# Performance work log

Measured on AMD Instinct MI355X. Metric: run time of the kernel, lower is better.

The kernel has to match this reference:

```python
import jax, jax.numpy as jnp
import numpy as np

NEG = -65504.0  # torch.finfo(float16).min
EPS = 1e-6

B, T, D = 2, 1024, 2048
H, HD = 16, 128          # n_head, head_dim
K = 128                  # dynamic_w_hidden_dim
IH = 1                   # dynamic_hidden_dim = H // squeeze_ratio


def _rope(x, freqs_cis):
    # x: [B,T,H,hd]; 'half' mode: first/second half are the rotation pair,
    # output is interleaved (stack(...,-1).flatten(3) in torch).
    half = x.shape[-1] // 2
    a, b = x[..., :half], x[..., half:]
    cos = freqs_cis[None, :, None, :, 0]
    sin = freqs_cis[None, :, None, :, 1]
    out = jnp.stack([a * cos - b * sin, b * cos + a * sin], axis=-1)
    return out.reshape(x.shape)


def _cross_head_proj(inputs, qw1, qw2, kw1, kw2, qdd, kdd):
    # inputs: [B,N,T,S]; qw1/qw2: [B,T,I,N]; kw1/kw2: [B,S,I,N]; qdd: [B,T,N]; kdd: [B,S,N]
    out = inputs
    out = out + jnp.einsum('bnts,btin,btim->bmts', inputs, qw1, qw2)
    out = out + jnp.einsum('bnts,bsin,bsim->bmts', inputs, kw1, kw2)
    out = out + inputs * jnp.swapaxes(qdd, 1, 2)[..., None]   # [B,N,T,1]
    out = out + inputs * jnp.swapaxes(kdd, 1, 2)[:, :, None, :]  # [B,N,1,S]
    return out


def setup_inputs() -> dict:
    key = jax.random.key(0)
    ks = jax.random.split(key, 7)
    x = jax.random.normal(ks[0], (B, T, D), jnp.float32)
    mask = jnp.tril(jnp.ones((1, 1, T, T), bool))  # causal
    # rotary tables: [T, hd/2, 2] (cos, sin)
    inv = 1.0 / (10000.0 ** (jnp.arange(0, HD, 2, dtype=jnp.float32) / HD))
    ang = jnp.arange(T, dtype=jnp.float32)[:, None] * inv[None, :]
    freqs_cis = jnp.stack([jnp.cos(ang), jnp.sin(ang)], axis=-1)
    s = 0.02
    wqkv = jax.random.normal(ks[1], (D, 3 * H * HD), jnp.float32) * s
    wo = jax.random.normal(ks[2], (H * HD, D), jnp.float32) * s
    dw1 = jax.random.normal(ks[3], (D, 4, K), jnp.float32) * s
    qkw = jax.random.normal(ks[4], (4, K, 2 * IH, H), jnp.float32) * s
    dd_w = jax.random.normal(ks[5], (D, 4 * H), jnp.float32) * s
    return {"x": x, "mask": mask, "freqs_cis": freqs_cis, "wqkv": wqkv,
            "wo": wo, "dw1": dw1, "qkw": qkw, "dd_w": dd_w}


def reference(x, mask, freqs_cis, wqkv, wo, dw1, qkw, dd_w):
    b, t, d = x.shape
    qkv = x @ wqkv
    q, k, v = jnp.split(qkv, [H * HD, 2 * H * HD], axis=-1)
    q = q.reshape(b, t, H, HD)
    k = k.reshape(b, t, H, HD)
    v = v.reshape(b, t, H, HD)
    q = _rope(q, freqs_cis)
    k = _rope(k, freqs_cis)
    q = jnp.swapaxes(q, 1, 2) * (HD ** -0.5)  # [B,H,T,hd]
    k = jnp.swapaxes(k, 1, 2)
    v = jnp.swapaxes(v, 1, 2)

    # ---- DynamicWeightProjection (G=1, squeezed) ----
    dw_hidden = jax.nn.gelu(jnp.einsum('btd,dck->btck', x, dw1), approximate=False)
    w = jnp.einsum('btck,ckim->btcim', dw_hidden, qkw)  # [B,T,4,2*IH,H]
    w1, w2 = w[..., :IH, :], w[..., IH:, :]
    w1 = w1 * jax.lax.rsqrt(jnp.mean(w1 * w1, axis=-1, keepdims=True) + EPS)
    pre_qw1, pre_kw1, post_qw1, post_kw1 = [w1[:, :, i] for i in range(4)]
    pre_qw2, pre_kw2, post_qw2, post_kw2 = [w2[:, :, i] for i in range(4)]
    dd = jnp.tanh(x @ dd_w).reshape(b, t, 4, H)
    pre_qdd, pre_kdd, post_qdd, post_kdd = [dd[:, :, i] for i in range(4)]

    # ---- attention with cross-head mixing ----
    logits = jnp.einsum('bhtd,bhsd->bhts', q, k)
    logits = _cross_head_proj(logits, pre_qw1, pre_qw2, pre_kw1, pre_kw2, pre_qdd, pre_kdd)
    logits = jnp.where(mask, logits, NEG)
    probs = jax.nn.softmax(logits, axis=-1)
    probs = _cross_head_proj(probs, post_qw1, post_qw2, post_kw1, post_kw2, post_qdd, post_kdd)
    o = jnp.einsum('bhts,bhsd->bhtd', probs, v)
    o = jnp.swapaxes(o, 1, 2).reshape(b, t, H * HD)
    return o @ wo
```

## Files before the change

kernel.cpp:

```cpp
#include <hip/hip_runtime.h>


typedef unsigned short u16;
typedef unsigned int u32;
typedef __attribute__((ext_vector_type(8))) short s16x8;
typedef __attribute__((ext_vector_type(4))) float f32x4;
typedef __attribute__((ext_vector_type(2))) float f32x2;
typedef __attribute__((ext_vector_type(2))) u16 u16x2;

#define DEV __device__ __forceinline__

DEV float bf2f(u16 u) { union { u32 u; float f; } a; a.u = ((u32)u) << 16; return a.f; }
DEV u16 f2bf(float f) {
  union { float f; u32 u; } a; a.f = f;
  u32 r = a.u + 0x7fffu + ((a.u >> 16) & 1u);
  return (u16)(r >> 16);
}

DEV void gload16(const void* g, void* l) {
  __builtin_amdgcn_global_load_lds((__attribute__((address_space(1))) void*)g,
                                   (__attribute__((address_space(3))) void*)l,
                                   16, 0, 0);
}

template <int OUTBF>
__global__ __launch_bounds__(256) void gemm_bt(
    const u16* __restrict__ A, const u16* __restrict__ B, void* __restrict__ Cp,
    int K, int lda, int ldb, int ldc,
    long sAb, long sBb, long sCb1, long sCb2, int CZ2, int cmode, int swz)
{
  int bx = blockIdx.x, by = blockIdx.y;
  if (swz) {
    int nx = gridDim.x;
    int fid = by * nx + bx;
    int cpx = (nx * gridDim.y) >> 3;
    int nid = (fid & 7) * cpx + (fid >> 3);
    bx = nid % nx; by = nid / nx;
  }
  if (cmode == 1 && bx > by) return;
  __shared__ u16 sA[128 * 64];
  __shared__ u16 sB[128 * 64];
  const int tid = threadIdx.x, wv = tid >> 6, ln = tid & 63;
  const int z = blockIdx.z;
  const u16* Ab = A + (size_t)z * sAb + (size_t)(by * 128) * lda;
  const u16* Bb = B + (size_t)z * sBb + (size_t)(bx * 128) * ldb;
  const int wr = (wv >> 1) * 64, wc = (wv & 1) * 64;
  const int Keff = (cmode == 2) ? min(K, (by + 1) * 128) : K;

  f32x4 acc[4][4];
#pragma unroll
  for (int m = 0; m < 4; ++m)
#pragma unroll
    for (int n = 0; n < 4; ++n) {
      f32x4 zz = {0.f, 0.f, 0.f, 0.f};
      acc[m][n] = zz;
    }

  int o_[4], r_[4], cb_[4];
#pragma unroll
  for (int i = 0; i < 4; ++i) {
    int o = (wv * 4 + i) * 1024 + ln * 16;
    o_[i] = o;
    int r = o >> 7;
    r_[i] = r;
    cb_[i] = (o & 127) ^ ((r & 7) << 4);
  }
  const int frswz = (ln & 7) << 4;
  const int fkcol = (ln >> 4) << 4;

  for (int k0 = 0; k0 < Keff; k0 += 64) {
    __syncthreads();
#pragma unroll
    for (int i = 0; i < 4; ++i)
      gload16(Ab + (size_t)r_[i] * lda + (k0 + (cb_[i] >> 1)), (char*)sA + o_[i]);
#pragma unroll
    for (int i = 0; i < 4; ++i)
      gload16(Bb + (size_t)r_[i] * ldb + (k0 + (cb_[i] >> 1)), (char*)sB + o_[i]);
    __syncthreads();

#pragma unroll
    for (int ks = 0; ks < 2; ++ks) {
      s16x8 av[4], bv[4];
#pragma unroll
      for (int m = 0; m < 4; ++m) {
        int row = wr + m * 16 + (ln & 15);
        int addr = row * 128 + ((ks * 64 + fkcol) ^ frswz);
        av[m] = *(const s16x8*)((const char*)sA + addr);
      }
#pragma unroll
      for (int n = 0; n < 4; ++n) {
        int row = wc + n * 16 + (ln & 15);
        int addr = row * 128 + ((ks * 64 + fkcol) ^ frswz);
        bv[n] = *(const s16x8*)((const char*)sB + addr);
      }
#pragma unroll
      for (int m = 0; m < 4; ++m)
#pragma unroll
        for (int n = 0; n < 4; ++n)
          acc[m][n] = __builtin_amdgcn_mfma_f32_16x16x32_bf16(av[m], bv[n], acc[m][n], 0, 0, 0);
    }
  }

  const size_t cbase = (size_t)(z / CZ2) * sCb1 + (size_t)(z % CZ2) * sCb2;
  const int r0 = by * 128 + wr + ((ln >> 4) << 2);
  const int c0 = bx * 128 + wc + (ln & 15);
#pragma unroll
  for (int m = 0; m < 4; ++m)
#pragma unroll
    for (int n = 0; n < 4; ++n)
#pragma unroll
      for (int j = 0; j < 4; ++j) {
        int row = r0 + m * 16 + j, col = c0 + n * 16;
        if (OUTBF)
          ((u16*)Cp)[cbase + (size_t)row * ldc + col] = f2bf(acc[m][n][j]);
        else
          ((float*)Cp)[cbase + (size_t)row * ldc + col] = acc[m][n][j];
      }
}

template <int INBF>
__global__ __launch_bounds__(256) void transpose_to_bf16(
    const void* __restrict__ srcv, u16* __restrict__ dst,
    int R, int C, int Cpad, int srcLd, long sSrc1, long sSrc2, int Z2, long sDst)
{
  __shared__ float tile[32][33];
  const int z = blockIdx.z, z1 = z / Z2, z2 = z % Z2;
  const size_t sbase = (size_t)z1 * sSrc1 + (size_t)z2 * sSrc2;
  u16* d = dst + (size_t)z * sDst;
  const int c0 = blockIdx.x * 32, r0 = blockIdx.y * 32;
  const int tx = threadIdx.x, ty = threadIdx.y;
#pragma unroll
  for (int i = 0; i < 4; ++i) {
    int r = r0 + ty + i * 8, c = c0 + tx;
    float v = 0.f;
    if (c < C && r < R) {
      if (INBF) v = bf2f(((const u16*)srcv)[sbase + (size_t)r * srcLd + c]);
      else      v = ((const float*)srcv)[sbase + (size_t)r * srcLd + c];
    }
    tile[ty + i * 8][tx] = v;
  }
  __syncthreads();
#pragma unroll
  for (int i = 0; i < 4; ++i) {
    int dr = c0 + ty + i * 8, dc = r0 + tx;
    if (dr < Cpad && dc < R) d[(size_t)dr * R + dc] = f2bf(tile[tx][ty + i * 8]);
  }
}

__global__ void cvt_f32_bf16_k(const float* __restrict__ src, u16* __restrict__ dst, int n4) {
  int i = blockIdx.x * 256 + threadIdx.x;
  if (i >= n4) return;
  const float4 v = ((const float4*)src)[i];
  u16* o = dst + (size_t)i * 4;
  o[0] = f2bf(v.x); o[1] = f2bf(v.y); o[2] = f2bf(v.z); o[3] = f2bf(v.w);
}

__global__ __launch_bounds__(256) void rope_k(
    const u16* __restrict__ qkvb, const float* __restrict__ fc,
    u16* __restrict__ qb, u16* __restrict__ kb)
{
  const int bt = blockIdx.x, b = bt >> 10, t = bt & 1023;
  const u16* row = qkvb + (size_t)bt * 6144;
  const float SC = 0.08838834764831845f;
#pragma unroll
  for (int it = 0; it < 4; ++it) {
    int idx = threadIdx.x + it * 256;
    int h = idx >> 6, j = idx & 63;
    float c = fc[(t * 64 + j) * 2], sn = fc[(t * 64 + j) * 2 + 1];
    float qa = bf2f(row[h * 128 + j]), qbv = bf2f(row[h * 128 + 64 + j]);
    float ka = bf2f(row[2048 + h * 128 + j]), kbv = bf2f(row[2048 + h * 128 + 64 + j]);
    size_t o = ((size_t)(b * 16 + h) * 1024 + t) * 128 + 2 * j;
    qb[o]     = f2bf((qa * c - qbv * sn) * SC);
    qb[o + 1] = f2bf((qbv * c + qa * sn) * SC);
    kb[o]     = f2bf(ka * c - kbv * sn);
    kb[o + 1] = f2bf(kbv * c + ka * sn);
  }
}

__global__ __launch_bounds__(128) void gelu_k(float* __restrict__ hm) {
  int bt = blockIdx.x, tid = threadIdx.x;
  float* p = hm + (size_t)bt * 640 + tid * 4;
  float4 v = *(float4*)p;
  v.x = 0.5f * v.x * (1.f + erff(v.x * 0.70710678118654752f));
  v.y = 0.5f * v.y * (1.f + erff(v.y * 0.70710678118654752f));
  v.z = 0.5f * v.z * (1.f + erff(v.z * 0.70710678118654752f));
  v.w = 0.5f * v.w * (1.f + erff(v.w * 0.70710678118654752f));
  *(float4*)p = v;
}

__global__ __launch_bounds__(64) void wproj_k(
    const float* __restrict__ hid, const float* __restrict__ qkw,
    float* __restrict__ w1a, float* __restrict__ w2a, float* __restrict__ kpT)
{
  const int bt = blockIdx.x, ln = threadIdx.x;
  const int c = ln >> 4, m = ln & 15;
  const int b = bt >> 10, t = bt & 1023;
  const float* hp = hid + (size_t)bt * 640 + c * 128;
  const float* Wp = qkw + (size_t)c * 4096 + m;
  float w1 = 0.f, w2 = 0.f;
  for (int k = 0; k < 128; ++k) {
    float hv = hp[k];
    w1 += hv * Wp[k * 32];
    w2 += hv * Wp[k * 32 + 16];
  }
  float ss = w1 * w1;
  ss += __shfl_xor(ss, 1); ss += __shfl_xor(ss, 2);
  ss += __shfl_xor(ss, 4); ss += __shfl_xor(ss, 8);
  float nrm = rsqrtf(ss * (1.f / 16.f) + 1e-6f);
  float w1n = w1 * nrm;
  size_t o = (size_t)bt * 64 + c * 16 + m;
  w1a[o] = w1n;
  w2a[o] = w2;
  size_t kb = (size_t)b * 98304 + (size_t)m * 1024 + t;
  if (c == 1) { kpT[kb] = w1n; kpT[kb + 16384] = w2; }
  if (c == 3) { kpT[kb + 49152] = w1n; kpT[kb + 65536] = w2; }
}

__global__ __launch_bounds__(64) void dd_k(const float* __restrict__ hm,
                                           float* __restrict__ dda, float* __restrict__ kpT) {
  int bt = blockIdx.x, ln = threadIdx.x;
  int c = ln >> 4, m = ln & 15;
  int b = bt >> 10, t = bt & 1023;
  float v = tanhf(hm[(size_t)bt * 640 + 512 + ln]);
  dda[(size_t)bt * 64 + ln] = v;
  size_t kb = (size_t)b * 98304 + (size_t)m * 1024 + t;
  if (c == 1) kpT[kb + 32768] = v;
  if (c == 3) kpT[kb + 81920] = v;
}

__global__ __launch_bounds__(512, 4) void proj_softmax_k(
    const float* __restrict__ L, u16* __restrict__ P,
    const float* __restrict__ w1a, const float* __restrict__ w2a,
    const float* __restrict__ dda, const float* __restrict__ kparT)
{
  const int t = blockIdx.x, b = blockIdx.y;
  const int tid = threadIdx.x, wv = tid >> 6, ln = tid & 63;
  const int s0 = tid * 2;
  const bool live = (s0 <= t);

  __shared__ float qpar[6][16];
  __shared__ float red2[16][8];
  __shared__ float rzf[16];
  if (tid < 96) {
    int a = tid >> 4, hh = tid & 15;
    const float* sp = (a == 0 || a == 3) ? w1a : ((a == 1 || a == 4) ? w2a : dda);
    int cc = (a < 3) ? 0 : 2;
    qpar[a][hh] = sp[(size_t)(b * 1024 + t) * 64 + cc * 16 + hh];
  }
  __syncthreads();

  const float* kp = kparT + (size_t)b * 98304 + s0;
  float v[16][2];
  const size_t lbase = ((size_t)(b * 16) * 1024 + t) * 1024 + s0;

  if (live) {
#pragma unroll
    for (int h = 0; h < 16; ++h) {
      f32x2 d = *(const f32x2*)(L + lbase + (size_t)h * 1048576);
      v[h][0] = d[0]; v[h][1] = d[1];
    }
    float dq0 = 0.f, dq1 = 0.f, dk0 = 0.f, dk1 = 0.f;
#pragma unroll
    for (int h = 0; h < 16; ++h) {
      f32x2 k1 = *(const f32x2*)(kp + h * 1024);
      dq0 += v[h][0] * qpar[0][h]; dq1 += v[h][1] * qpar[0][h];
      dk0 += v[h][0] * k1[0];      dk1 += v[h][1] * k1[1];
    }
    const bool ok1 = (s0 + 1 <= t);
#pragma unroll
    for (int h = 0; h < 16; ++h) {
      f32x2 k2 = *(const f32x2*)(kp + 16384 + h * 1024);
      f32x2 kd = *(const f32x2*)(kp + 32768 + h * 1024);
      float a0 = v[h][0] * (1.f + qpar[2][h] + kd[0]) + qpar[1][h] * dq0 + k2[0] * dk0;
      float a1 = v[h][1] * (1.f + qpar[2][h] + kd[1]) + qpar[1][h] * dq1 + k2[1] * dk1;
      v[h][0] = __expf(a0);
      v[h][1] = ok1 ? __expf(a1) : 0.f;
    }
  }

#pragma unroll
  for (int h = 0; h < 16; ++h) {
    float x = live ? (v[h][0] + v[h][1]) : 0.f;
#pragma unroll
    for (int off = 32; off > 0; off >>= 1) x += __shfl_xor(x, off);
    if (ln == 0) red2[h][wv] = x;
  }
  __syncthreads();
  if (tid < 16)
    rzf[tid] = 1.f / (((red2[tid][0] + red2[tid][1]) + (red2[tid][2] + red2[tid][3])) +
                      ((red2[tid][4] + red2[tid][5]) + (red2[tid][6] + red2[tid][7])));
  __syncthreads();

  const size_t pbase = ((size_t)(b * 16) * 1024 + t) * 1024 + s0;
  if (live) {
    float pdq0 = 0.f, pdq1 = 0.f, pdk0 = 0.f, pdk1 = 0.f;
#pragma unroll
    for (int h = 0; h < 16; ++h) {
      float rz = rzf[h];
      f32x2 k1 = *(const f32x2*)(kp + 49152 + h * 1024);
      float p0 = v[h][0] * rz, p1 = v[h][1] * rz;
      v[h][0] = p0; v[h][1] = p1;
      pdq0 += p0 * qpar[3][h]; pdq1 += p1 * qpar[3][h];
      pdk0 += p0 * k1[0];      pdk1 += p1 * k1[1];
    }
#pragma unroll
    for (int h = 0; h < 16; ++h) {
      f32x2 k2 = *(const f32x2*)(kp + 65536 + h * 1024);
      f32x2 kd = *(const f32x2*)(kp + 81920 + h * 1024);
      u16x2 pk;
      pk[0] = f2bf(v[h][0] * (1.f + qpar[5][h] + kd[0]) + qpar[4][h] * pdq0 + k2[0] * pdk0);
      pk[1] = f2bf(v[h][1] * (1.f + qpar[5][h] + kd[1]) + qpar[4][h] * pdq1 + k2[1] * pdk1);
      *(u16x2*)(P + pbase + (size_t)h * 1048576) = pk;
    }
  } else {
    u16x2 z2 = {0, 0};
#pragma unroll
    for (int h = 0; h < 16; ++h)
      *(u16x2*)(P + pbase + (size_t)h * 1048576) = z2;
  }
}

extern "C" void kernel_launch(void* const* d_in, const int* in_sizes, int n_in,
                              void* d_out, int out_size, void* d_ws, size_t ws_size,
                              hipStream_t stream)
{
  (void)in_sizes; (void)n_in; (void)out_size; (void)ws_size;
  const float* x    = (const float*)d_in[0];
  const float* fc   = (const float*)d_in[2];
  const float* wqkv = (const float*)d_in[3];
  const float* wo   = (const float*)d_in[4];
  const float* dw1  = (const float*)d_in[5];
  const float* qkw  = (const float*)d_in[6];
  const float* ddw  = (const float*)d_in[7];
  float* out = (float*)d_out;
  char* w = (char*)d_ws;

  u16*   woT   = (u16*)(w + 0);
  u16*   qb    = (u16*)(w + 8388608);
  u16*   kb    = (u16*)(w + 16777216);
  u16*   vT    = (u16*)(w + 25165824);
  u16*   obf   = (u16*)(w + 33554432);
  float* w1a   = (float*)(w + 41943040);
  float* w2a   = (float*)(w + 42467328);
  float* dda   = (float*)(w + 42991616);
  const size_t TB = 43515904;
  u16*   xb    = (u16*)(w + TB);
  u16*   wqkvT = (u16*)(w + TB + 8388608);
  u16*   dwddT = (u16*)(w + TB + 33554432);
  u16*   qkvb  = (u16*)(w + TB + 36175872);
  float* hidm  = (float*)(w + TB + 61341696);
  float* L     = (float*)(w + TB);
  u16*   P     = (u16*)(w + TB + 134217728);
  float* kparT = (float*)(w + 244842496);

  cvt_f32_bf16_k<<<4096, 256, 0, stream>>>(x, xb, 1048576);
  transpose_to_bf16<0><<<dim3(192, 64, 1), dim3(32, 8), 0, stream>>>(wqkv, wqkvT, 2048, 6144, 6144, 6144, 0, 0, 1, 0);
  transpose_to_bf16<0><<<dim3(16, 64, 1),  dim3(32, 8), 0, stream>>>(dw1,  dwddT, 2048, 512,  512,  512,  0, 0, 1, 0);
  transpose_to_bf16<0><<<dim3(4, 64, 1),   dim3(32, 8), 0, stream>>>(ddw,  dwddT + 512 * 2048, 2048, 64, 128, 64, 0, 0, 1, 0);
  transpose_to_bf16<0><<<dim3(64, 64, 1),  dim3(32, 8), 0, stream>>>(wo,   woT,   2048, 2048, 2048, 2048, 0, 0, 1, 0);

  gemm_bt<1><<<dim3(48, 16, 1), 256, 0, stream>>>(xb, wqkvT, qkvb, 2048, 2048, 2048, 6144, 0, 0, 0, 0, 1, 0, 1);
  rope_k<<<2048, 256, 0, stream>>>(qkvb, fc, qb, kb);
  transpose_to_bf16<1><<<dim3(4, 32, 32), dim3(32, 8), 0, stream>>>(qkvb + 4096, vT, 1024, 128, 128, 6144, 6291456, 128, 16, 131072);

  gemm_bt<0><<<dim3(5, 16, 1), 256, 0, stream>>>(xb, dwddT, hidm, 2048, 2048, 2048, 640, 0, 0, 0, 0, 1, 0, 0);
  gelu_k<<<2048, 128, 0, stream>>>(hidm);
  wproj_k<<<2048, 64, 0, stream>>>(hidm, qkw, w1a, w2a, kparT);
  dd_k<<<2048, 64, 0, stream>>>(hidm, dda, kparT);

  gemm_bt<0><<<dim3(8, 8, 32), 256, 0, stream>>>(qb, kb, L, 128, 128, 128, 1024, 131072, 131072, 1048576, 0, 1, 1, 0);
  proj_softmax_k<<<dim3(1024, 2, 1), 512, 0, stream>>>(L, P, w1a, w2a, dda, kparT);
  gemm_bt<1><<<dim3(1, 8, 32), 256, 0, stream>>>(P, vT, obf, 1024, 1024, 1024, 2048, 1048576, 131072, 2097152, 128, 16, 2, 0);

  gemm_bt<0><<<dim3(16, 16, 1), 256, 0, stream>>>(obf, woT, out, 2048, 2048, 2048, 2048, 0, 0, 0, 0, 1, 0, 1);
}
```

Baseline: 336.9 us.

## Fuse dynamic-weight GEMM into QKV GEMM and process two query rows per softmax block

The dw1 and dd_w weight transposes now sit next to wqkv, so one GEMM with N=6784 produces QKV plus the dynamic hidden pre-activations in bf16. This removes the separate small GEMM launch and its poor occupancy, and gelu, wproj and dd now read that bf16 output. The proj_softmax kernel now handles two query rows per block, which halves the block count and reuses the key-side parameter loads across both rows. In exchange, the hidden activations are rounded to bf16 before gelu, and each thread holds more registers.

```diff
diff --git a/kernel.cpp b/kernel.cpp
--- a/kernel.cpp
+++ b/kernel.cpp
@@ -7,6 +7,7 @@
 typedef __attribute__((ext_vector_type(4))) float f32x4;
 typedef __attribute__((ext_vector_type(2))) float f32x2;
 typedef __attribute__((ext_vector_type(2))) u16 u16x2;
+typedef __attribute__((ext_vector_type(8))) u16 u16x8;
 
 #define DEV __device__ __forceinline__
 
@@ -156,11 +157,11 @@
 }
 
 __global__ __launch_bounds__(256) void rope_k(
-    const u16* __restrict__ qkvb, const float* __restrict__ fc,
+    const u16* __restrict__ qkvm, const float* __restrict__ fc,
     u16* __restrict__ qb, u16* __restrict__ kb)
 {
   const int bt = blockIdx.x, b = bt >> 10, t = bt & 1023;
-  const u16* row = qkvb + (size_t)bt * 6144;
+  const u16* row = qkvm + (size_t)bt * 6784;
   const float SC = 0.08838834764831845f;
 #pragma unroll
   for (int it = 0; it < 4; ++it) {
@@ -177,29 +178,31 @@
   }
 }
 
-__global__ __launch_bounds__(128) void gelu_k(float* __restrict__ hm) {
+__global__ __launch_bounds__(64) void gelu_bf16_k(u16* __restrict__ qm) {
   int bt = blockIdx.x, tid = threadIdx.x;
-  float* p = hm + (size_t)bt * 640 + tid * 4;
-  float4 v = *(float4*)p;
-  v.x = 0.5f * v.x * (1.f + erff(v.x * 0.70710678118654752f));
-  v.y = 0.5f * v.y * (1.f + erff(v.y * 0.70710678118654752f));
-  v.z = 0.5f * v.z * (1.f + erff(v.z * 0.70710678118654752f));
-  v.w = 0.5f * v.w * (1.f + erff(v.w * 0.70710678118654752f));
-  *(float4*)p = v;
+  u16* p = qm + (size_t)bt * 6784 + 6144 + tid * 8;
+  u16x8 v = *(u16x8*)p;
+#pragma unroll
+  for (int i = 0; i < 8; ++i) {
+    float f = bf2f(v[i]);
+    f = 0.5f * f * (1.f + erff(f * 0.70710678118654752f));
+    v[i] = f2bf(f);
+  }
+  *(u16x8*)p = v;
 }
 
 __global__ __launch_bounds__(64) void wproj_k(
-    const float* __restrict__ hid, const float* __restrict__ qkw,
+    const u16* __restrict__ qkvm, const float* __restrict__ qkw,
     float* __restrict__ w1a, float* __restrict__ w2a, float* __restrict__ kpT)
 {
   const int bt = blockIdx.x, ln = threadIdx.x;
   const int c = ln >> 4, m = ln & 15;
   const int b = bt >> 10, t = bt & 1023;
-  const float* hp = hid + (size_t)bt * 640 + c * 128;
+  const u16* hp = qkvm + (size_t)bt * 6784 + 6144 + c * 128;
   const float* Wp = qkw + (size_t)c * 4096 + m;
   float w1 = 0.f, w2 = 0.f;
   for (int k = 0; k < 128; ++k) {
-    float hv = hp[k];
+    float hv = bf2f(hp[k]);
     w1 += hv * Wp[k * 32];
     w2 += hv * Wp[k * 32 + 16];
   }
@@ -216,12 +219,12 @@
   if (c == 3) { kpT[kb + 49152] = w1n; kpT[kb + 65536] = w2; }
 }
 
-__global__ __launch_bounds__(64) void dd_k(const float* __restrict__ hm,
+__global__ __launch_bounds__(64) void dd_k(const u16* __restrict__ qkvm,
                                            float* __restrict__ dda, float* __restrict__ kpT) {
   int bt = blockIdx.x, ln = threadIdx.x;
   int c = ln >> 4, m = ln & 15;
   int b = bt >> 10, t = bt & 1023;
-  float v = tanhf(hm[(size_t)bt * 640 + 512 + ln]);
+  float v = tanhf(bf2f(qkvm[(size_t)bt * 6784 + 6656 + ln]));
   dda[(size_t)bt * 64 + ln] = v;
   size_t kb = (size_t)b * 98304 + (size_t)m * 1024 + t;
   if (c == 1) kpT[kb + 32768] = v;
@@ -233,90 +236,121 @@
     const float* __restrict__ w1a, const float* __restrict__ w2a,
     const float* __restrict__ dda, const float* __restrict__ kparT)
 {
-  const int t = blockIdx.x, b = blockIdx.y;
+  const int t0 = blockIdx.x * 2, b = blockIdx.y;
   const int tid = threadIdx.x, wv = tid >> 6, ln = tid & 63;
   const int s0 = tid * 2;
-  const bool live = (s0 <= t);
-
-  __shared__ float qpar[6][16];
-  __shared__ float red2[16][8];
-  __shared__ float rzf[16];
-  if (tid < 96) {
-    int a = tid >> 4, hh = tid & 15;
+  const bool liveB = (s0 <= t0 + 1);
+
+  __shared__ float qpar[2][6][16];
+  __shared__ float red2[2][16][8];
+  __shared__ float rzf[2][16];
+  if (tid < 192) {
+    int tt = (tid >= 96) ? 1 : 0, u = tid - tt * 96;
+    int a = u >> 4, hh = u & 15;
     const float* sp = (a == 0 || a == 3) ? w1a : ((a == 1 || a == 4) ? w2a : dda);
     int cc = (a < 3) ? 0 : 2;
-    qpar[a][hh] = sp[(size_t)(b * 1024 + t) * 64 + cc * 16 + hh];
+    qpar[tt][a][hh] = sp[(size_t)(b * 1024 + t0 + tt) * 64 + cc * 16 + hh];
   }
   __syncthreads();
 
   const float* kp = kparT + (size_t)b * 98304 + s0;
-  float v[16][2];
-  const size_t lbase = ((size_t)(b * 16) * 1024 + t) * 1024 + s0;
-
-  if (live) {
-#pragma unroll
-    for (int h = 0; h < 16; ++h) {
-      f32x2 d = *(const f32x2*)(L + lbase + (size_t)h * 1048576);
-      v[h][0] = d[0]; v[h][1] = d[1];
-    }
-    float dq0 = 0.f, dq1 = 0.f, dk0 = 0.f, dk1 = 0.f;
+  float vA[16][2], vB[16][2];
+  const size_t lbaseA = ((size_t)(b * 16) * 1024 + t0) * 1024 + s0;
+  const size_t lbaseB = lbaseA + 1024;
+
+  if (liveB) {
+#pragma unroll
+    for (int h = 0; h < 16; ++h) {
+      f32x2 dA = *(const f32x2*)(L + lbaseA + (size_t)h * 1048576);
+      f32x2 dB = *(const f32x2*)(L + lbaseB + (size_t)h * 1048576);
+      vA[h][0] = dA[0]; vA[h][1] = dA[1];
+      vB[h][0] = dB[0]; vB[h][1] = dB[1];
+    }
+    float dqA0 = 0.f, dqA1 = 0.f, dkA0 = 0.f, dkA1 = 0.f;
+    float dqB0 = 0.f, dqB1 = 0.f, dkB0 = 0.f, dkB1 = 0.f;
 #pragma unroll
     for (int h = 0; h < 16; ++h) {
       f32x2 k1 = *(const f32x2*)(kp + h * 1024);
-      dq0 += v[h][0] * qpar[0][h]; dq1 += v[h][1] * qpar[0][h];
-      dk0 += v[h][0] * k1[0];      dk1 += v[h][1] * k1[1];
-    }
-    const bool ok1 = (s0 + 1 <= t);
+      dqA0 += vA[h][0] * qpar[0][0][h]; dqA1 += vA[h][1] * qpar[0][0][h];
+      dkA0 += vA[h][0] * k1[0];         dkA1 += vA[h][1] * k1[1];
+      dqB0 += vB[h][0] * qpar[1][0][h]; dqB1 += vB[h][1] * qpar[1][0][h];
+      dkB0 += vB[h][0] * k1[0];         dkB1 += vB[h][1] * k1[1];
+    }
+    const bool okA0 = (s0 <= t0), okA1 = (s0 + 1 <= t0), okB1 = (s0 + 1 <= t0 + 1);
 #pragma unroll
     for (int h = 0; h < 16; ++h) {
       f32x2 k2 = *(const f32x2*)(kp + 16384 + h * 1024);
       f32x2 kd = *(const f32x2*)(kp + 32768 + h * 1024);
-      float a0 = v[h][0] * (1.f + qpar[2][h] + kd[0]) + qpar[1][h] * dq0 + k2[0] * dk0;
-      float a1 = v[h][1] * (1.f + qpar[2][h] + kd[1]) + qpar[1][h] * dq1 + k2[1] * dk1;
-      v[h][0] = __expf(a0);
-      v[h][1] = ok1 ? __expf(a1) : 0.f;
+      float aA0 = vA[h][0] * (1.f + qpar[0][2][h] + kd[0]) + qpar[0][1][h] * dqA0 + k2[0] * dkA0;
+      float aA1 = vA[h][1] * (1.f + qpar[0][2][h] + kd[1]) + qpar[0][1][h] * dqA1 + k2[1] * dkA1;
+      float aB0 = vB[h][0] * (1.f + qpar[1][2][h] + kd[0]) + qpar[1][1][h] * dqB0 + k2[0] * dkB0;
+      float aB1 = vB[h][1] * (1.f + qpar[1][2][h] + kd[1]) + qpar[1][1][h] * dqB1 + k2[1] * dkB1;
+      vA[h][0] = okA0 ? __expf(aA0) : 0.f;
+      vA[h][1] = okA1 ? __expf(aA1) : 0.f;
+      vB[h][0] = __expf(aB0);
+      vB[h][1] = okB1 ? __expf(aB1) : 0.f;
+    }
+  } else {
+#pragma unroll
+    for (int h = 0; h < 16; ++h) {
+      vA[h][0] = 0.f; vA[h][1] = 0.f; vB[h][0] = 0.f; vB[h][1] = 0.f;
     }
   }
 
 #pragma unroll
   for (int h = 0; h < 16; ++h) {
-    float x = live ? (v[h][0] + v[h][1]) : 0.f;
-#pragma unroll
-    for (int off = 32; off > 0; off >>= 1) x += __shfl_xor(x, off);
-    if (ln == 0) red2[h][wv] = x;
+    float xA = vA[h][0] + vA[h][1];
+    float xB = vB[h][0] + vB[h][1];
+#pragma unroll
+    for (int off = 32; off > 0; off >>= 1) {
+      xA += __shfl_xor(xA, off);
+      xB += __shfl_xor(xB, off);
+    }
+    if (ln == 0) { red2[0][h][wv] = xA; red2[1][h][wv] = xB; }
   }
   __syncthreads();
-  if (tid < 16)
-    rzf[tid] = 1.f / (((red2[tid][0] + red2[tid][1]) + (red2[tid][2] + red2[tid][3])) +
-                      ((red2[tid][4] + red2[tid][5]) + (red2[tid][6] + red2[tid][7])));
+  if (tid < 32) {
+    int tt = tid >> 4, h = tid & 15;
+    rzf[tt][h] = 1.f / (((red2[tt][h][0] + red2[tt][h][1]) + (red2[tt][h][2] + red2[tt][h][3])) +
+                        ((red2[tt][h][4] + red2[tt][h][5]) + (red2[tt][h][6] + red2[tt][h][7])));
+  }
   __syncthreads();
 
-  const size_t pbase = ((size_t)(b * 16) * 1024 + t) * 1024 + s0;
-  if (live) {
-    float pdq0 = 0.f, pdq1 = 0.f, pdk0 = 0.f, pdk1 = 0.f;
-#pragma unroll
-    for (int h = 0; h < 16; ++h) {
-      float rz = rzf[h];
+  const size_t pbaseA = lbaseA, pbaseB = lbaseB;
+  if (liveB) {
+    float pdqA0 = 0.f, pdqA1 = 0.f, pdkA0 = 0.f, pdkA1 = 0.f;
+    float pdqB0 = 0.f, pdqB1 = 0.f, pdkB0 = 0.f, pdkB1 = 0.f;
+#pragma unroll
+    for (int h = 0; h < 16; ++h) {
       f32x2 k1 = *(const f32x2*)(kp + 49152 + h * 1024);
-      float p0 = v[h][0] * rz, p1 = v[h][1] * rz;
-      v[h][0] = p0; v[h][1] = p1;
-      pdq0 += p0 * qpar[3][h]; pdq1 += p1 * qpar[3][h];
-      pdk0 += p0 * k1[0];      pdk1 += p1 * k1[1];
+      float rzA = rzf[0][h], rzB = rzf[1][h];
+      float pA0 = vA[h][0] * rzA, pA1 = vA[h][1] * rzA;
+      float pB0 = vB[h][0] * rzB, pB1 = vB[h][1] * rzB;
+      vA[h][0] = pA0; vA[h][1] = pA1; vB[h][0] = pB0; vB[h][1] = pB1;
+      pdqA0 += pA0 * qpar[0][3][h]; pdqA1 += pA1 * qpar[0][3][h];
+      pdkA0 += pA0 * k1[0];         pdkA1 += pA1 * k1[1];
+      pdqB0 += pB0 * qpar[1][3][h]; pdqB1 += pB1 * qpar[1][3][h];
+      pdkB0 += pB0 * k1[0];         pdkB1 += pB1 * k1[1];
     }
 #pragma unroll
     for (int h = 0; h < 16; ++h) {
       f32x2 k2 = *(const f32x2*)(kp + 65536 + h * 1024);
       f32x2 kd = *(const f32x2*)(kp + 81920 + h * 1024);
-      u16x2 pk;
-      pk[0] = f2bf(v[h][0] * (1.f + qpar[5][h] + kd[0]) + qpar[4][h] * pdq0 + k2[0] * pdk0);
-      pk[1] = f2bf(v[h][1] * (1.f + qpar[5][h] + kd[1]) + qpar[4][h] * pdq1 + k2[1] * pdk1);
-      *(u16x2*)(P + pbase + (size_t)h * 1048576) = pk;
+      u16x2 pkA, pkB;
+      pkA[0] = f2bf(vA[h][0] * (1.f + qpar[0][5][h] + kd[0]) + qpar[0][4][h] * pdqA0 + k2[0] * pdkA0);
+      pkA[1] = f2bf(vA[h][1] * (1.f + qpar[0][5][h] + kd[1]) + qpar[0][4][h] * pdqA1 + k2[1] * pdkA1);
+      pkB[0] = f2bf(vB[h][0] * (1.f + qpar[1][5][h] + kd[0]) + qpar[1][4][h] * pdqB0 + k2[0] * pdkB0);
+      pkB[1] = f2bf(vB[h][1] * (1.f + qpar[1][5][h] + kd[1]) + qpar[1][4][h] * pdqB1 + k2[1] * pdkB1);
+      *(u16x2*)(P + pbaseA + (size_t)h * 1048576) = pkA;
+      *(u16x2*)(P + pbaseB + (size_t)h * 1048576) = pkB;
     }
   } else {
     u16x2 z2 = {0, 0};
 #pragma unroll
-    for (int h = 0; h < 16; ++h)
-      *(u16x2*)(P + pbase + (size_t)h * 1048576) = z2;
+    for (int h = 0; h < 16; ++h) {
+      *(u16x2*)(P + pbaseA + (size_t)h * 1048576) = z2;
+      *(u16x2*)(P + pbaseB + (size_t)h * 1048576) = z2;
+    }
   }
 }
 
@@ -345,31 +379,28 @@
   float* dda   = (float*)(w + 42991616);
   const size_t TB = 43515904;
   u16*   xb    = (u16*)(w + TB);
-  u16*   wqkvT = (u16*)(w + TB + 8388608);
-  u16*   dwddT = (u16*)(w + TB + 33554432);
-  u16*   qkvb  = (u16*)(w + TB + 36175872);
-  float* hidm  = (float*)(w + TB + 61341696);
+  u16*   wallT = (u16*)(w + TB + 8388608);
+  u16*   qkvm  = (u16*)(w + TB + 36175872);
   float* L     = (float*)(w + TB);
   u16*   P     = (u16*)(w + TB + 134217728);
   float* kparT = (float*)(w + 244842496);
 
   cvt_f32_bf16_k<<<4096, 256, 0, stream>>>(x, xb, 1048576);
-  transpose_to_bf16<0><<<dim3(192, 64, 1), dim3(32, 8), 0, stream>>>(wqkv, wqkvT, 2048, 6144, 6144, 6144, 0, 0, 1, 0);
-  transpose_to_bf16<0><<<dim3(16, 64, 1),  dim3(32, 8), 0, stream>>>(dw1,  dwddT, 2048, 512,  512,  512,  0, 0, 1, 0);
-  transpose_to_bf16<0><<<dim3(4, 64, 1),   dim3(32, 8), 0, stream>>>(ddw,  dwddT + 512 * 2048, 2048, 64, 128, 64, 0, 0, 1, 0);
-  transpose_to_bf16<0><<<dim3(64, 64, 1),  dim3(32, 8), 0, stream>>>(wo,   woT,   2048, 2048, 2048, 2048, 0, 0, 1, 0);
-
-  gemm_bt<1><<<dim3(48, 16, 1), 256, 0, stream>>>(xb, wqkvT, qkvb, 2048, 2048, 2048, 6144, 0, 0, 0, 0, 1, 0, 1);
-  rope_k<<<2048, 256, 0, stream>>>(qkvb, fc, qb, kb);
-  transpose_to_bf16<1><<<dim3(4, 32, 32), dim3(32, 8), 0, stream>>>(qkvb + 4096, vT, 1024, 128, 128, 6144, 6291456, 128, 16, 131072);
-
-  gemm_bt<0><<<dim3(5, 16, 1), 256, 0, stream>>>(xb, dwddT, hidm, 2048, 2048, 2048, 640, 0, 0, 0, 0, 1, 0, 0);
-  gelu_k<<<2048, 128, 0, stream>>>(hidm);
-  wproj_k<<<2048, 64, 0, stream>>>(hidm, qkw, w1a, w2a, kparT);
-  dd_k<<<2048, 64, 0, stream>>>(hidm, dda, kparT);
+  transpose_to_bf16<0><<<dim3(192, 64, 1), dim3(32, 8), 0, stream>>>(wqkv, wallT, 2048, 6144, 6144, 6144, 0, 0, 1, 0);
+  transpose_to_bf16<0><<<dim3(16, 64, 1),  dim3(32, 8), 0, stream>>>(dw1,  wallT + (size_t)6144 * 2048, 2048, 512, 512, 512, 0, 0, 1, 0);
+  transpose_to_bf16<0><<<dim3(4, 64, 1),   dim3(32, 8), 0, stream>>>(ddw,  wallT + (size_t)6656 * 2048, 2048, 64, 128, 64, 0, 0, 1, 0);
+  transpose_to_bf16<0><<<dim3(64, 64, 1),  dim3(32, 8), 0, stream>>>(wo,   woT, 2048, 2048, 2048, 2048, 0, 0, 1, 0);
+
+  gemm_bt<1><<<dim3(53, 16, 1), 256, 0, stream>>>(xb, wallT, qkvm, 2048, 2048, 2048, 6784, 0, 0, 0, 0, 1, 0, 1);
+  rope_k<<<2048, 256, 0, stream>>>(qkvm, fc, qb, kb);
+  transpose_to_bf16<1><<<dim3(4, 32, 32), dim3(32, 8), 0, stream>>>(qkvm + 4096, vT, 1024, 128, 128, 6784, 6946816, 128, 16, 131072);
+
+  gelu_bf16_k<<<2048, 64, 0, stream>>>(qkvm);
+  wproj_k<<<2048, 64, 0, stream>>>(qkvm, qkw, w1a, w2a, kparT);
+  dd_k<<<2048, 64, 0, stream>>>(qkvm, dda, kparT);
 
   gemm_bt<0><<<dim3(8, 8, 32), 256, 0, stream>>>(qb, kb, L, 128, 128, 128, 1024, 131072, 131072, 1048576, 0, 1, 1, 0);
-  proj_softmax_k<<<dim3(1024, 2, 1), 512, 0, stream>>>(L, P, w1a, w2a, dda, kparT);
+  proj_softmax_k<<<dim3(512, 2, 1), 512, 0, stream>>>(L, P, w1a, w2a, dda, kparT);
   gemm_bt<1><<<dim3(1, 8, 32), 256, 0, stream>>>(P, vT, obf, 1024, 1024, 1024, 2048, 1048576, 131072, 2097152, 128, 16, 2, 0);
 
   gemm_bt<0><<<dim3(16, 16, 1), 256, 0, stream>>>(obf, woT, out, 2048, 2048, 2048, 2048, 0, 0, 0, 0, 1, 0, 1);
```

Result: slower. 471.6 us (+40.0%).
